# Performance work log

Hardware: AMD Instinct MI355X
Metric: run time of the kernel (lower is better)

## Reference

```python
import jax, jax.numpy as jnp
import numpy as np

D_MODEL = 1024
N_HEADS = 16
D_HEAD = D_MODEL // N_HEADS
D_FF = 4 * D_MODEL
B, T = 2, 2048
LN_EPS = 1e-5


def layer_norm(x, g, b):
    mu = jnp.mean(x, axis=-1, keepdims=True)
    var = jnp.mean(jnp.square(x - mu), axis=-1, keepdims=True)
    return (x - mu) * jax.lax.rsqrt(var + LN_EPS) * g + b


def setup_inputs() -> dict:
    key = jax.random.key(0)
    ks = jax.random.split(key, 8)
    s = lambda fan: 1.0 / np.sqrt(fan)
    return {
        "x": jax.random.normal(ks[0], (B, T, D_MODEL), dtype=jnp.float32),
        "ln1_g": jnp.ones((D_MODEL,), jnp.float32),
        "ln1_b": jnp.zeros((D_MODEL,), jnp.float32),
        "Wqkv": jax.random.normal(ks[1], (D_MODEL, 3 * D_MODEL), jnp.float32) * s(D_MODEL),
        "Wout": jax.random.normal(ks[2], (D_MODEL, D_MODEL), jnp.float32) * s(D_MODEL),
        "ln2_g": jnp.ones((D_MODEL,), jnp.float32),
        "ln2_b": jnp.zeros((D_MODEL,), jnp.float32),
        "W1": jax.random.normal(ks[3], (D_MODEL, D_FF), jnp.float32) * s(D_MODEL),
        "b1": jnp.zeros((D_FF,), jnp.float32),
        "W2": jax.random.normal(ks[4], (D_FF, D_MODEL), jnp.float32) * s(D_FF),
        "b2": jnp.zeros((D_MODEL,), jnp.float32),
    }


def attention(x, Wqkv, Wout):
    Bx, Tx, C = x.shape
    qkv = x @ Wqkv  # [B,T,3C]
    q, k, v = jnp.split(qkv, 3, axis=-1)
    q = q.reshape(Bx, Tx, N_HEADS, D_HEAD)
    k = k.reshape(Bx, Tx, N_HEADS, D_HEAD)
    v = v.reshape(Bx, Tx, N_HEADS, D_HEAD)
    scores = jnp.einsum('bqhd,bkhd->bhqk', q, k) / np.sqrt(D_HEAD).astype(np.float32)
    causal = jnp.tril(jnp.ones((Tx, Tx), dtype=bool))
    scores = jnp.where(causal, scores, -jnp.inf)
    attn = jax.nn.softmax(scores, axis=-1)
    out = jnp.einsum('bhqk,bkhd->bqhd', attn, v).reshape(Bx, Tx, C)
    return out @ Wout


def reference(x, ln1_g, ln1_b, Wqkv, Wout, ln2_g, ln2_b, W1, b1, W2, b2):
    x = x + attention(layer_norm(x, ln1_g, ln1_b), Wqkv, Wout)
    h = layer_norm(x, ln2_g, ln2_b)
    h = jax.nn.gelu(h @ W1 + b1, approximate=False) @ W2 + b2
    return x + h
```

## Files before the change

kernel.cpp:

```cpp
#include <hip/hip_runtime.h>
#include <math.h>

typedef __bf16 bf16;
typedef __bf16 bf16x4 __attribute__((ext_vector_type(4)));
typedef __bf16 bf16x8 __attribute__((ext_vector_type(8)));
typedef float  f32x4  __attribute__((ext_vector_type(4)));

#define MFMA16(a,b,c) __builtin_amdgcn_mfma_f32_16x16x32_bf16((a),(b),(c),0,0,0)

static __device__ __forceinline__ bf16x8 combine8(const bf16* plo, const bf16* phi) {
  bf16x4 lo = *(const bf16x4*)plo;
  bf16x4 hi = *(const bf16x4*)phi;
  return __builtin_shufflevector(lo, hi, 0, 1, 2, 3, 4, 5, 6, 7);
}

__global__ __launch_bounds__(256) void transpose_cast(const float* __restrict__ W,
                                                      bf16* __restrict__ WT,
                                                      int K, int N) {
  __shared__ float t[32][33];
  int n0 = blockIdx.x * 32, k0 = blockIdx.y * 32;
  int tx = threadIdx.x, ty = threadIdx.y;
#pragma unroll
  for (int i = 0; i < 32; i += 8)
    t[ty + i][tx] = W[(size_t)(k0 + ty + i) * N + n0 + tx];
  __syncthreads();
#pragma unroll
  for (int i = 0; i < 32; i += 8)
    WT[(size_t)(n0 + ty + i) * K + k0 + tx] = (bf16)t[tx][ty + i];
}

__global__ __launch_bounds__(256) void ln_kernel(const float* __restrict__ X,
                                                 const float* __restrict__ g,
                                                 const float* __restrict__ bta,
                                                 bf16* __restrict__ out) {
  int row  = blockIdx.x * 4 + (threadIdx.x >> 6);
  int lane = threadIdx.x & 63;
  const float4* x4 = (const float4*)(X + (size_t)row * 1024);
  float4 v[4];
  float s = 0.f, ss = 0.f;
#pragma unroll
  for (int i = 0; i < 4; ++i) {
    v[i] = x4[i * 64 + lane];
    s  += v[i].x + v[i].y + v[i].z + v[i].w;
    ss += v[i].x * v[i].x + v[i].y * v[i].y + v[i].z * v[i].z + v[i].w * v[i].w;
  }
#pragma unroll
  for (int off = 1; off < 64; off <<= 1) {
    s  += __shfl_xor(s, off, 64);
    ss += __shfl_xor(ss, off, 64);
  }
  float mu  = s * (1.0f / 1024.0f);
  float var = ss * (1.0f / 1024.0f) - mu * mu;
  float rs  = rsqrtf(var + 1e-5f);
  bf16* orow = out + (size_t)row * 1024;
#pragma unroll
  for (int i = 0; i < 4; ++i) {
    int c = i * 256 + lane * 4;
    bf16x4 pk;
    pk[0] = (bf16)((v[i].x - mu) * rs * g[c + 0] + bta[c + 0]);
    pk[1] = (bf16)((v[i].y - mu) * rs * g[c + 1] + bta[c + 1]);
    pk[2] = (bf16)((v[i].z - mu) * rs * g[c + 2] + bta[c + 2]);
    pk[3] = (bf16)((v[i].w - mu) * rs * g[c + 3] + bta[c + 3]);
    *(bf16x4*)(orow + c) = pk;
  }
}

template <int ROWS>
static __device__ __forceinline__ void stage_lds(const bf16* __restrict__ gbase,
                                                 int gstride, int k0,
                                                 unsigned char* lds_base,
                                                 int wv, int lane) {
#pragma unroll
  for (int i = 0; i < ROWS / 32; ++i) {
    int r = wv * (ROWS / 4) + i * 8 + (lane >> 3);
    int u = (lane & 7) ^ (r & 7);
    const bf16* src = gbase + (size_t)r * gstride + k0 + u * 8;
    __builtin_amdgcn_global_load_lds(
        (const __attribute__((address_space(1))) void*)src,
        (__attribute__((address_space(3))) void*)(lds_base + (wv * (ROWS / 4) + i * 8) * 128),
        16, 0, 0);
  }
}

static __device__ __forceinline__ bf16x8 frag_ld(const unsigned char* lds_base,
                                                 int r, int u) {
  return *(const bf16x8*)(lds_base + r * 128 + (((u ^ (r & 7)) & 7) << 4));
}

template <int EPI, int BM, int DBUF>
__global__ __launch_bounds__(256) void gemm_bt(const bf16* __restrict__ A,
                                               const bf16* __restrict__ BT,
                                               int K, int N, int gx,
                                               const float* __restrict__ bias,
                                               const float* __restrict__ res,
                                               bf16* __restrict__ outb,
                                               float* __restrict__ outf) {
  constexpr int MI = BM / 32;
  constexpr int TILE = (BM + 128) * 128;
  __shared__ unsigned char smem[TILE * (DBUF ? 2 : 1)];
  int nwg = gridDim.x, bid = blockIdx.x;
  int nb = (bid & 7) * (nwg >> 3) + (bid >> 3);
  int bx = nb % gx, by = nb / gx;
  int brow = by * BM, bcol = bx * 128;
  int tid = threadIdx.x, wv = tid >> 6, lane = tid & 63;
  int l15 = lane & 15, l4 = lane >> 4;
  int wm = wv >> 1, wn = wv & 1;
  f32x4 acc[MI][4] = {};
  const bf16* Ab = A + (size_t)brow * K;
  const bf16* Bb = BT + (size_t)bcol * K;

  int cur = 0;
  if (DBUF) {
    stage_lds<BM>(Ab, K, 0, smem, wv, lane);
    stage_lds<128>(Bb, K, 0, smem + BM * 128, wv, lane);
    __syncthreads();
  }
  for (int k0 = 0; k0 < K; k0 += 64) {
    unsigned char* sc;
    if (DBUF) {
      sc = smem + cur * TILE;
      if (k0 + 64 < K) {
        unsigned char* sn = smem + (cur ^ 1) * TILE;
        stage_lds<BM>(Ab, K, k0 + 64, sn, wv, lane);
        stage_lds<128>(Bb, K, k0 + 64, sn + BM * 128, wv, lane);
      }
    } else {
      sc = smem;
      stage_lds<BM>(Ab, K, k0, sc, wv, lane);
      stage_lds<128>(Bb, K, k0, sc + BM * 128, wv, lane);
      __syncthreads();
    }
    unsigned char* As = sc;
    unsigned char* Bs = sc + BM * 128;
#pragma unroll
    for (int ks = 0; ks < 2; ++ks) {
      bf16x8 af[MI], bfr[4];
#pragma unroll
      for (int mi = 0; mi < MI; ++mi)
        af[mi] = frag_ld(As, wm * (BM / 2) + mi * 16 + l15, ks * 4 + l4);
#pragma unroll
      for (int ni = 0; ni < 4; ++ni)
        bfr[ni] = frag_ld(Bs, wn * 64 + ni * 16 + l15, ks * 4 + l4);
#pragma unroll
      for (int mi = 0; mi < MI; ++mi)
#pragma unroll
        for (int ni = 0; ni < 4; ++ni)
          acc[mi][ni] = MFMA16(af[mi], bfr[ni], acc[mi][ni]);
    }
    __syncthreads();
    cur ^= 1;
  }
#pragma unroll
  for (int mi = 0; mi < MI; ++mi) {
#pragma unroll
    for (int ni = 0; ni < 4; ++ni) {
      int col  = bcol + wn * 64 + ni * 16 + l15;
      int row0 = brow + wm * (BM / 2) + mi * 16 + l4 * 4;
#pragma unroll
      for (int r = 0; r < 4; ++r) {
        int row = row0 + r;
        float v = acc[mi][ni][r];
        if (EPI == 1) {
          v += bias[col];
          v = 0.5f * v * (1.0f + erff(v * 0.70710678118654752f));
        }
        if (EPI == 2) v += res[(size_t)row * N + col];
        if (EPI == 3) v += bias[col] + res[(size_t)row * N + col];
        if (EPI == 0 || EPI == 1) outb[(size_t)row * N + col] = (bf16)v;
        else                      outf[(size_t)row * N + col] = v;
      }
    }
  }
}

__global__ __launch_bounds__(256) void pack_kv(const bf16* __restrict__ qkv,
                                               bf16* __restrict__ kpack,
                                               bf16* __restrict__ vpack) {
  int blk = blockIdx.x;
  int wv = threadIdx.x >> 6, lane = threadIdx.x & 63;
  int l15 = lane & 15, l4 = lane >> 4;
  int ch = (blk & 15) * 4 + wv;
  int bh = blk >> 4;
  int b = bh >> 4, h = bh & 15;
  const bf16* kq = qkv + (size_t)b * 2048 * 3072 + 1024 + h * 64;
  const bf16* vq = kq + 1024;
#pragma unroll
  for (int fr = 0; fr < 4; ++fr) {
    int key = ch * 32 + ((fr >> 1) << 4) + l15;
    int dbase = ((fr & 1) << 5) + l4 * 4;
    bf16x8 v = combine8(kq + (size_t)key * 3072 + dbase,
                        kq + (size_t)key * 3072 + dbase + 16);
    *(bf16x8*)(kpack + ((size_t)(bh * 64 + ch) * 4 + fr) * 512 + lane * 8) = v;
  }
#pragma unroll
  for (int db = 0; db < 4; ++db) {
    int d = db * 16 + l15;
    bf16x8 v;
#pragma unroll
    for (int j = 0; j < 8; ++j) {
      int key = ch * 32 + l4 * 4 + (j & 3) + ((j >> 2) << 4);
      v[j] = vq[(size_t)key * 3072 + d];
    }
    *(bf16x8*)(vpack + ((size_t)(bh * 64 + ch) * 4 + db) * 512 + lane * 8) = v;
  }
}

static __device__ __forceinline__ void proc_chunk(
    const bf16x8* __restrict__ kf, const bf16x8* __restrict__ vf,
    const bf16x8 (* __restrict__ qf)[2], f32x4 (* __restrict__ o)[4],
    float* __restrict__ lsum, bool diag, int l15, int l4) {
  const float SC = 0.125f * 1.4426950408889634f;
#pragma unroll
  for (int f = 0; f < 2; ++f) {
    f32x4 c0 = {0.f, 0.f, 0.f, 0.f}, c1 = {0.f, 0.f, 0.f, 0.f};
    c0 = MFMA16(kf[0], qf[f][0], c0);
    c0 = MFMA16(kf[1], qf[f][1], c0);
    c1 = MFMA16(kf[2], qf[f][0], c1);
    c1 = MFMA16(kf[3], qf[f][1], c1);
    bf16x8 pf;
    float ls = 0.f;
#pragma unroll
    for (int r = 0; r < 4; ++r) {
      float e0 = __builtin_amdgcn_exp2f(c0[r] * SC);
      float e1 = __builtin_amdgcn_exp2f(c1[r] * SC);
      if (diag) {
        int qg = f * 16 + l15;
        int key = l4 * 4 + r;
        if (key > qg)      e0 = 0.f;
        if (key + 16 > qg) e1 = 0.f;
      }
      ls += e0 + e1;
      pf[r]     = (bf16)e0;
      pf[4 + r] = (bf16)e1;
    }
    lsum[f] += ls;
    o[f][0] = MFMA16(vf[0], pf, o[f][0]);
    o[f][1] = MFMA16(vf[1], pf, o[f][1]);
    o[f][2] = MFMA16(vf[2], pf, o[f][2]);
    o[f][3] = MFMA16(vf[3], pf, o[f][3]);
  }
}

__global__ __launch_bounds__(256) void attn_kernel(const bf16* __restrict__ qkv,
                                                   const bf16* __restrict__ kpack,
                                                   const bf16* __restrict__ vpack,
                                                   bf16* __restrict__ attn_out) {
  __shared__ float mbuf[3 * 68 * 64];
  int bid = blockIdx.x;
  int nb = (bid & 7) * 128 + (bid >> 3);
  int bh = nb >> 5, j = nb & 31;
  int b = bh >> 4, h = bh & 15;
  int wv = threadIdx.x >> 6, lane = threadIdx.x & 63;
  int l15 = lane & 15, l4 = lane >> 4;
  int qc[2] = {j, 63 - j};
  const bf16* base = qkv + (size_t)b * 2048 * 3072;
  int d0 = l4 * 4;
  bf16x8 qf[2][2][2];
#pragma unroll
  for (int c = 0; c < 2; ++c)
#pragma unroll
    for (int f = 0; f < 2; ++f) {
      const bf16* qp = base + (size_t)(qc[c] * 32 + f * 16 + l15) * 3072 + h * 64;
      qf[c][f][0] = combine8(qp + d0,      qp + d0 + 16);
      qf[c][f][1] = combine8(qp + d0 + 32, qp + d0 + 48);
    }
  const bf16* kp0 = kpack + (size_t)bh * 64 * 2048 + lane * 8;
  const bf16* vp0 = vpack + (size_t)bh * 64 * 2048 + lane * 8;

  f32x4 o[2][2][4] = {};
  float lsum[2][2] = {};

  for (int ch = wv; ch <= qc[1]; ch += 4) {
    const bf16* kp = kp0 + (size_t)ch * 2048;
    const bf16* vp = vp0 + (size_t)ch * 2048;
    bf16x8 kf[4], vf[4];
    kf[0] = *(const bf16x8*)(kp);
    kf[1] = *(const bf16x8*)(kp + 512);
    kf[2] = *(const bf16x8*)(kp + 1024);
    kf[3] = *(const bf16x8*)(kp + 1536);
    vf[0] = *(const bf16x8*)(vp);
    vf[1] = *(const bf16x8*)(vp + 512);
    vf[2] = *(const bf16x8*)(vp + 1024);
    vf[3] = *(const bf16x8*)(vp + 1536);
    if (ch <= qc[0])
      proc_chunk(kf, vf, qf[0], o[0], lsum[0], ch == qc[0], l15, l4);
    proc_chunk(kf, vf, qf[1], o[1], lsum[1], ch == qc[1], l15, l4);
  }

  if (wv > 0) {
    float* dst = mbuf + (wv - 1) * 68 * 64 + lane;
#pragma unroll
    for (int c = 0; c < 2; ++c)
#pragma unroll
      for (int f = 0; f < 2; ++f) {
#pragma unroll
        for (int db = 0; db < 4; ++db)
#pragma unroll
          for (int r = 0; r < 4; ++r)
            dst[(c * 32 + f * 16 + db * 4 + r) * 64] = o[c][f][db][r];
        dst[(64 + c * 2 + f) * 64] = lsum[c][f];
      }
  }
  __syncthreads();
  if (wv == 0) {
#pragma unroll
    for (int w = 0; w < 3; ++w) {
      const float* src = mbuf + w * 68 * 64 + lane;
#pragma unroll
      for (int c = 0; c < 2; ++c)
#pragma unroll
        for (int f = 0; f < 2; ++f) {
#pragma unroll
          for (int db = 0; db < 4; ++db)
#pragma unroll
            for (int r = 0; r < 4; ++r)
              o[c][f][db][r] += src[(c * 32 + f * 16 + db * 4 + r) * 64];
          lsum[c][f] += src[(64 + c * 2 + f) * 64];
        }
    }
#pragma unroll
    for (int c = 0; c < 2; ++c)
#pragma unroll
      for (int f = 0; f < 2; ++f) {
        float l = lsum[c][f];
        l += __shfl_xor(l, 16, 64);
        l += __shfl_xor(l, 32, 64);
        float inv = 1.0f / l;
#pragma unroll
        for (int db = 0; db < 4; ++db)
#pragma unroll
          for (int r = 0; r < 4; ++r) {
            int d = db * 16 + l4 * 4 + r;
            attn_out[(size_t)(b * 2048 + qc[c] * 32 + f * 16 + l15) * 1024 +
                     h * 64 + d] = (bf16)(o[c][f][db][r] * inv);
          }
      }
  }
}

extern "C" void kernel_launch(void* const* d_in, const int* in_sizes, int n_in,
                              void* d_out, int out_size, void* d_ws, size_t ws_size,
                              hipStream_t stream) {
  const float* x     = (const float*)d_in[0];
  const float* ln1g  = (const float*)d_in[1];
  const float* ln1b  = (const float*)d_in[2];
  const float* Wqkv  = (const float*)d_in[3];
  const float* Wout  = (const float*)d_in[4];
  const float* ln2g  = (const float*)d_in[5];
  const float* ln2b  = (const float*)d_in[6];
  const float* W1    = (const float*)d_in[7];
  const float* b1    = (const float*)d_in[8];
  const float* W2    = (const float*)d_in[9];
  const float* b2    = (const float*)d_in[10];
  float* out = (float*)d_out;

  char* p = (char*)d_ws;
  bf16* WqkvT = (bf16*)p; p += (size_t)3072 * 1024 * 2;
  bf16* WoutT = (bf16*)p; p += (size_t)1024 * 1024 * 2;
  bf16* W1T   = (bf16*)p; p += (size_t)4096 * 1024 * 2;
  bf16* W2T   = (bf16*)p; p += (size_t)1024 * 4096 * 2;
  bf16* hbuf  = (bf16*)p; p += (size_t)4096 * 1024 * 2;
  bf16* aobuf = (bf16*)p; p += (size_t)4096 * 1024 * 2;
  bf16* big   = (bf16*)p; p += (size_t)4096 * 4096 * 2;

  bf16* kpack = big + (size_t)4096 * 3072;
  bf16* vpack = hbuf;

  dim3 tb(32, 8);
  transpose_cast<<<dim3(96, 32),  tb, 0, stream>>>(Wqkv, WqkvT, 1024, 3072);
  transpose_cast<<<dim3(32, 32),  tb, 0, stream>>>(Wout, WoutT, 1024, 1024);
  transpose_cast<<<dim3(128, 32), tb, 0, stream>>>(W1,   W1T,   1024, 4096);
  transpose_cast<<<dim3(32, 128), tb, 0, stream>>>(W2,   W2T,   4096, 1024);

  ln_kernel<<<1024, 256, 0, stream>>>(x, ln1g, ln1b, hbuf);
  gemm_bt<0, 128, 0><<<768, 256, 0, stream>>>(hbuf, WqkvT, 1024, 3072, 24,
                                              nullptr, nullptr, big, nullptr);
  pack_kv<<<512, 256, 0, stream>>>(big, kpack, vpack);
  attn_kernel<<<1024, 256, 0, stream>>>(big, kpack, vpack, aobuf);
  gemm_bt<2, 64, 1><<<512, 256, 0, stream>>>(aobuf, WoutT, 1024, 1024, 8,
                                             nullptr, x, nullptr, out);
  ln_kernel<<<1024, 256, 0, stream>>>(out, ln2g, ln2b, hbuf);
  gemm_bt<1, 128, 0><<<1024, 256, 0, stream>>>(hbuf, W1T, 1024, 4096, 32,
                                               b1, nullptr, big, nullptr);
  gemm_bt<3, 64, 1><<<512, 256, 0, stream>>>(big, W2T, 4096, 1024, 8,
                                             b2, out, nullptr, out);
}
```

Measured before the change: 235.8 us.

## Double-buffer all GEMMs, precompute staging pointers, use tanh GELU

Every GEMM now double-buffers its LDS tiles, including the BM=128 QKV and W1 GEMMs that were single-buffered, so global-to-LDS loads overlap MFMA work. Per-thread global source pointers are computed once outside the K loop rather than on every stage. The exact erf GELU in the W1 epilogue is replaced by a tanh approximation built on hardware exp2 and rcp. Doubling LDS for the BM=128 kernels may lower occupancy, and the tanh GELU departs numerically from the reference's exact erf GELU.

```diff
diff --git a/kernel.cpp b/kernel.cpp
--- a/kernel.cpp
+++ b/kernel.cpp
@@ -65,21 +65,15 @@
   }
 }
 
-template <int ROWS>
-static __device__ __forceinline__ void stage_lds(const bf16* __restrict__ gbase,
-                                                 int gstride, int k0,
-                                                 unsigned char* lds_base,
-                                                 int wv, int lane) {
-#pragma unroll
-  for (int i = 0; i < ROWS / 32; ++i) {
-    int r = wv * (ROWS / 4) + i * 8 + (lane >> 3);
-    int u = (lane & 7) ^ (r & 7);
-    const bf16* src = gbase + (size_t)r * gstride + k0 + u * 8;
+template <int NR>
+static __device__ __forceinline__ void stage2(const bf16* const* srcs, int koff,
+                                              unsigned char* lds_base, int wv) {
+#pragma unroll
+  for (int i = 0; i < NR; ++i)
     __builtin_amdgcn_global_load_lds(
-        (const __attribute__((address_space(1))) void*)src,
-        (__attribute__((address_space(3))) void*)(lds_base + (wv * (ROWS / 4) + i * 8) * 128),
+        (const __attribute__((address_space(1))) void*)(srcs[i] + koff),
+        (__attribute__((address_space(3))) void*)(lds_base + (wv * (NR * 8) + i * 8) * 128),
         16, 0, 0);
-  }
 }
 
 static __device__ __forceinline__ bf16x8 frag_ld(const unsigned char* lds_base,
@@ -87,7 +81,15 @@
   return *(const bf16x8*)(lds_base + r * 128 + (((u ^ (r & 7)) & 7) << 4));
 }
 
-template <int EPI, int BM, int DBUF>
+static __device__ __forceinline__ float gelu_tanh(float v) {
+  float t = 0.7978845608028654f * (v + 0.044715f * v * v * v);
+  t = fminf(t, 15.0f);
+  float e = __builtin_amdgcn_exp2f(2.8853900817779268f * t);
+  float th = (e - 1.0f) * __builtin_amdgcn_rcpf(e + 1.0f);
+  return 0.5f * v * (1.0f + th);
+}
+
+template <int EPI, int BM>
 __global__ __launch_bounds__(256) void gemm_bt(const bf16* __restrict__ A,
                                                const bf16* __restrict__ BT,
                                                int K, int N, int gx,
@@ -96,8 +98,9 @@
                                                bf16* __restrict__ outb,
                                                float* __restrict__ outf) {
   constexpr int MI = BM / 32;
+  constexpr int ANR = BM / 32;
   constexpr int TILE = (BM + 128) * 128;
-  __shared__ unsigned char smem[TILE * (DBUF ? 2 : 1)];
+  __shared__ unsigned char smem[TILE * 2];
   int nwg = gridDim.x, bid = blockIdx.x;
   int nb = (bid & 7) * (nwg >> 3) + (bid >> 3);
   int bx = nb % gx, by = nb / gx;
@@ -106,29 +109,28 @@
   int l15 = lane & 15, l4 = lane >> 4;
   int wm = wv >> 1, wn = wv & 1;
   f32x4 acc[MI][4] = {};
-  const bf16* Ab = A + (size_t)brow * K;
-  const bf16* Bb = BT + (size_t)bcol * K;
-
+
+  int sr = lane >> 3;
+  int su = (lane & 7) ^ sr;
+  const bf16* aptr[ANR];
+#pragma unroll
+  for (int i = 0; i < ANR; ++i)
+    aptr[i] = A + (size_t)(brow + wv * (ANR * 8) + i * 8 + sr) * K + su * 8;
+  const bf16* bptr[4];
+#pragma unroll
+  for (int i = 0; i < 4; ++i)
+    bptr[i] = BT + (size_t)(bcol + wv * 32 + i * 8 + sr) * K + su * 8;
+
+  stage2<ANR>(aptr, 0, smem, wv);
+  stage2<4>(bptr, 0, smem + BM * 128, wv);
+  __syncthreads();
   int cur = 0;
-  if (DBUF) {
-    stage_lds<BM>(Ab, K, 0, smem, wv, lane);
-    stage_lds<128>(Bb, K, 0, smem + BM * 128, wv, lane);
-    __syncthreads();
-  }
   for (int k0 = 0; k0 < K; k0 += 64) {
-    unsigned char* sc;
-    if (DBUF) {
-      sc = smem + cur * TILE;
-      if (k0 + 64 < K) {
-        unsigned char* sn = smem + (cur ^ 1) * TILE;
-        stage_lds<BM>(Ab, K, k0 + 64, sn, wv, lane);
-        stage_lds<128>(Bb, K, k0 + 64, sn + BM * 128, wv, lane);
-      }
-    } else {
-      sc = smem;
-      stage_lds<BM>(Ab, K, k0, sc, wv, lane);
-      stage_lds<128>(Bb, K, k0, sc + BM * 128, wv, lane);
-      __syncthreads();
+    unsigned char* sc = smem + cur * TILE;
+    if (k0 + 64 < K) {
+      unsigned char* sn = smem + (cur ^ 1) * TILE;
+      stage2<ANR>(aptr, k0 + 64, sn, wv);
+      stage2<4>(bptr, k0 + 64, sn + BM * 128, wv);
     }
     unsigned char* As = sc;
     unsigned char* Bs = sc + BM * 128;
@@ -162,7 +164,7 @@
         float v = acc[mi][ni][r];
         if (EPI == 1) {
           v += bias[col];
-          v = 0.5f * v * (1.0f + erff(v * 0.70710678118654752f));
+          v = gelu_tanh(v);
         }
         if (EPI == 2) v += res[(size_t)row * N + col];
         if (EPI == 3) v += bias[col] + res[(size_t)row * N + col];
@@ -373,15 +375,15 @@
   transpose_cast<<<dim3(32, 128), tb, 0, stream>>>(W2,   W2T,   4096, 1024);
 
   ln_kernel<<<1024, 256, 0, stream>>>(x, ln1g, ln1b, hbuf);
-  gemm_bt<0, 128, 0><<<768, 256, 0, stream>>>(hbuf, WqkvT, 1024, 3072, 24,
-                                              nullptr, nullptr, big, nullptr);
+  gemm_bt<0, 128><<<768, 256, 0, stream>>>(hbuf, WqkvT, 1024, 3072, 24,
+                                           nullptr, nullptr, big, nullptr);
   pack_kv<<<512, 256, 0, stream>>>(big, kpack, vpack);
   attn_kernel<<<1024, 256, 0, stream>>>(big, kpack, vpack, aobuf);
-  gemm_bt<2, 64, 1><<<512, 256, 0, stream>>>(aobuf, WoutT, 1024, 1024, 8,
-                                             nullptr, x, nullptr, out);
+  gemm_bt<2, 64><<<512, 256, 0, stream>>>(aobuf, WoutT, 1024, 1024, 8,
+                                          nullptr, x, nullptr, out);
   ln_kernel<<<1024, 256, 0, stream>>>(out, ln2g, ln2b, hbuf);
-  gemm_bt<1, 128, 0><<<1024, 256, 0, stream>>>(hbuf, W1T, 1024, 4096, 32,
-                                               b1, nullptr, big, nullptr);
-  gemm_bt<3, 64, 1><<<512, 256, 0, stream>>>(big, W2T, 4096, 1024, 8,
-                                             b2, out, nullptr, out);
-}
+  gemm_bt<1, 128><<<1024, 256, 0, stream>>>(hbuf, W1T, 1024, 4096, 32,
+                                            b1, nullptr, big, nullptr);
+  gemm_bt<3, 64><<<512, 256, 0, stream>>>(big, W2T, 4096, 1024, 8,
+                                          b2, out, nullptr, out);
+}
```

After: 217.1 us. -7.9%, faster.
